# Performance work log

Hardware: AMD Instinct MI355X
Metric: run time of the kernel (lower is better)

Reference implementation:

```python
import jax, jax.numpy as jnp
import numpy as np

N = 65536          # nodes
D = 64             # nclasses / head dim
H = 1              # num_heads (forward math requires H == 1)
NITER = 4
NITER_ATTN = 4
KHOP = 2           # npow_attn(=1, hard-coded) + 1
R = 1024           # row-chunk size in residual loss
DEG = 8            # out-degree before symmetrization


def setup_inputs():
    rng = np.random.default_rng(0)
    cols0 = rng.integers(0, N, size=N * DEG).astype(np.int32)
    rows0 = np.repeat(np.arange(N, dtype=np.int32), DEG)
    loop = np.arange(N, dtype=np.int32)
    rows = np.concatenate([rows0, cols0, loop])           # symmetrized + self-loops (A + I)
    cols = np.concatenate([cols0, rows0, loop])
    deg = np.bincount(rows, minlength=N).astype(np.float32)
    vals = (1.0 / np.sqrt(deg[rows] * deg[cols])).astype(np.float32)  # D^-1/2 (A+I) D^-1/2
    key = jax.random.key(0)
    ks = jax.random.split(key, 8)
    sc = 1.0 / np.sqrt(D)
    return {
        "local_preds": jax.random.normal(ks[0], (N, D), jnp.float32),
        "idx": jnp.arange(N, dtype=jnp.int32),
        "adj_rows": jnp.asarray(rows),
        "adj_cols": jnp.asarray(cols),
        "adj_vals": jnp.asarray(vals),
        "Wq_w": jax.random.normal(ks[1], (H * D, D), jnp.float32) * sc,
        "Wq_b": jax.random.normal(ks[2], (H * D,), jnp.float32) * sc,
        "Wk_w": jax.random.normal(ks[3], (H * D, D), jnp.float32) * sc,
        "Wk_b": jax.random.normal(ks[4], (H * D,), jnp.float32) * sc,
        "lin1_w": jax.random.normal(ks[5], (1, NITER), jnp.float32) * sc,
        "lin2_w": jax.random.normal(ks[6], (1, NITER_ATTN), jnp.float32) * sc,
    }


def _spmm(rows, cols, vals, x):
    # sparse (A+I)_norm @ x via gather + segment-sum
    return jax.ops.segment_sum(vals[:, None] * x[cols], rows, num_segments=N)


def _fro(x):
    return jnp.sqrt(jnp.sum(x * x))


def _on_attn(qn, kn, vs, n_norm):
    # On_attention_conv with pre-normalized qn/kn, K_hop = KHOP
    new_vs = vs
    for _ in range(KHOP):
        kv = jnp.einsum('lhm,lhd->hmd', kn, new_vs)
        new_vs = jnp.einsum('nhm,hmd->nhd', qn, kv)
    new_vs = new_vs + vs.sum(axis=0)[None]           # + vs_sum broadcast over rows
    normz = jnp.einsum('nhm,hm->nh', qn, kn.sum(axis=0))[..., None] + n_norm
    return new_vs / normz


def _forward(local_preds, adj_rows, adj_cols, adj_vals, Wq_w, Wq_b, Wk_w, Wk_b, lin1_w, lin2_w):
    preds = local_preds
    query = (preds @ Wq_w.T + Wq_b).reshape(N, H, D)
    key_t = (preds @ Wk_w.T + Wk_b).reshape(N, H, D)
    qn = query / _fro(query)   # global-Frobenius normalization (as in torch.norm(qs, p=2))
    kn = key_t / _fro(key_t)
    beta = lin2_w[0]           # [NITER_ATTN]
    alph = lin1_w[0]           # [NITER]

    # main Hop-Stack iteration (H == 1 collapses the head broadcasts)
    M_list = [preds]
    tmp = preds
    for _ in range(1, NITER):
        qk_list = [tmp]
        qk_tmp = tmp
        for _ in range(1, NITER_ATTN):
            qk_tmp = _on_attn(qn, kn, qk_tmp[:, None, :], N).mean(axis=1)
            qk_list.append(qk_tmp)
        mix = jnp.einsum('k,knd->nd', beta, jnp.stack(qk_list))
        tmp = _spmm(adj_rows, adj_cols, adj_vals, mix)
        M_list.append(tmp)
    preds_out = jnp.einsum('k,knd->nd', alph, jnp.stack(M_list))

    # residual loss (torch.no_grad, N > r branch), computed in closed form per row-chunk
    m2 = [query.mean(axis=1)]
    t = query.mean(axis=1)
    for _ in range(2, NITER_ATTN):
        o = _on_attn(qn, kn, t[:, None, :], N).mean(axis=1)
        t = _spmm(adj_rows, adj_cols, adj_vals, o)
        m2.append(t)
    gq = jnp.einsum('k,knd->nd', beta[1:], jnp.stack(m2))[:, None, :]  # GraphA_q [N,H,D]
    c = N // R
    s = jnp.sqrt(jnp.sum(gq.reshape(c, -1) ** 2, axis=1))       # per-chunk Frobenius norm of qs
    row_chunk = jnp.arange(N) // R
    qn2 = gq * (1.0 / s)[row_chunk][:, None, None]
    normz = jnp.einsum('nhm,hm->nh', qn2, kn.sum(axis=0)) + R   # [N,H]
    G = jnp.einsum('lhm,lhp->hmp', kn, kn)                      # key gram [H,D,D]
    # ||attn||_F^2 summed over all chunks, without materializing [R,H,N]
    t1 = jnp.sum(jnp.einsum('nhm,hmp,nhp->nh', qn2, G, qn2) / normz ** 2)
    c0 = beta[0] - 1.0
    dots = jnp.einsum('ehm,ehm->eh', qn2[adj_rows], kn[adj_cols])  # attn at sparse A entries
    t2 = 2.0 * c0 * jnp.sum(adj_vals[:, None] * dots / normz[adj_rows])
    t3 = c0 ** 2 * H * jnp.sum(adj_vals ** 2)
    loss = jnp.sqrt(t1 + t2 + t3)
    return preds_out, jax.lax.stop_gradient(loss)


def reference(local_preds, idx, adj_rows, adj_cols, adj_vals, Wq_w, Wq_b, Wk_w, Wk_b, lin1_w, lin2_w):
    del idx  # unused by the original forward body
    return _forward(local_preds, adj_rows, adj_cols, adj_vals, Wq_w, Wq_b, Wk_w, Wk_b, lin1_w, lin2_w)
```

## Files before the change

### kernel.cpp

```cpp
#include <hip/hip_runtime.h>

#define NN 65536
#define DD 64
#define ND (NN*DD)
#define E0 (NN*8)
#define B1 128
#define EPB (E0/B1)

enum {
  SM_ACC   = 0,
  SM_SCAL  = 4,
  SM_KSUM  = 24,
  SM_CHUNK = 96,
  SM_T2    = 160,
  SM_KQ    = 2208,
  SM_G     = SM_KQ + 4096,
  SM_C0    = SM_G + 4096,
  SM_H     = SM_C0 + 4240,
  SM_Z     = SM_H + 4096,
  SM_ZF    = SM_Z + 4160,
  SM_C     = SM_ZF + 4160,
  SM_CMIX  = SM_C + 4240,
  SM_CFIN  = SM_CMIX + 4240,
  SM_END   = SM_CFIN + 4240
};

#define GP 512
#define RP 512
#define QKP 1024
#define GRAM_STRIDE 12544

__device__ __forceinline__ void f4arr(float4 v, float* a){ a[0]=v.x; a[1]=v.y; a[2]=v.z; a[3]=v.w; }

__device__ __forceinline__ unsigned short f2bf(float f){
  union{float f;unsigned u;}v; v.f=f;
  unsigned r = v.u + 0x7fffu + ((v.u>>16)&1u);
  return (unsigned short)(r>>16);
}
__device__ __forceinline__ float bf2f(unsigned short h){
  union{unsigned u;float f;}v; v.u=((unsigned)h)<<16; return v.f;
}

__global__ __launch_bounds__(256,4) void k_qk(const float* __restrict__ preds,
    const float* __restrict__ Wq, const float* __restrict__ bq,
    const float* __restrict__ Wk, const float* __restrict__ bk,
    float* __restrict__ qout, float* __restrict__ kout, float* __restrict__ slab)
{
  __shared__ float sWq[64*68];
  __shared__ float sWk[64*68];
  __shared__ float sbq[64], sbk[64], sks[64];
  __shared__ float sred[8];
  int t = threadIdx.x;
  for (int i=t;i<4096;i+=256){ int d=i>>6, m=i&63; sWq[m*68+d]=Wq[i]; sWk[m*68+d]=Wk[i]; }
  if (t<64){ sbq[t]=bq[t]; sbk[t]=bk[t]; sks[t]=0.f; }
  __syncthreads();
  int td=t&15, g=t>>4, d0=td*4;
  int base = blockIdx.x*64;
  float aq[16], ak[16];
  #pragma unroll
  for (int i=0;i<4;i++)
    #pragma unroll
    for (int j=0;j<4;j++){ aq[i*4+j]=sbq[d0+j]; ak[i*4+j]=sbk[d0+j]; }
  const float4* pr0=(const float4*)(preds+(size_t)(base+g   )*DD);
  const float4* pr1=(const float4*)(preds+(size_t)(base+g+16)*DD);
  const float4* pr2=(const float4*)(preds+(size_t)(base+g+32)*DD);
  const float4* pr3=(const float4*)(preds+(size_t)(base+g+48)*DD);
  float4 pc0=pr0[0], pc1=pr1[0], pc2=pr2[0], pc3=pr3[0];
  for (int ms=0; ms<16; ms++){
    float4 pn0=pc0,pn1=pc1,pn2=pc2,pn3=pc3;
    if (ms<15){ pn0=pr0[ms+1]; pn1=pr1[ms+1]; pn2=pr2[ms+1]; pn3=pr3[ms+1]; }
    int m=ms*4;
    float wq[4][4], wk[4][4];
    #pragma unroll
    for (int k=0;k<4;k++){ f4arr(*(const float4*)&sWq[(m+k)*68+d0], wq[k]); f4arr(*(const float4*)&sWk[(m+k)*68+d0], wk[k]); }
    float p[4];
    f4arr(pc0,p);
    #pragma unroll
    for (int k=0;k<4;k++)
      #pragma unroll
      for (int j=0;j<4;j++){ aq[0*4+j]+=p[k]*wq[k][j]; ak[0*4+j]+=p[k]*wk[k][j]; }
    f4arr(pc1,p);
    #pragma unroll
    for (int k=0;k<4;k++)
      #pragma unroll
      for (int j=0;j<4;j++){ aq[1*4+j]+=p[k]*wq[k][j]; ak[1*4+j]+=p[k]*wk[k][j]; }
    f4arr(pc2,p);
    #pragma unroll
    for (int k=0;k<4;k++)
      #pragma unroll
      for (int j=0;j<4;j++){ aq[2*4+j]+=p[k]*wq[k][j]; ak[2*4+j]+=p[k]*wk[k][j]; }
    f4arr(pc3,p);
    #pragma unroll
    for (int k=0;k<4;k++)
      #pragma unroll
      for (int j=0;j<4;j++){ aq[3*4+j]+=p[k]*wq[k][j]; ak[3*4+j]+=p[k]*wk[k][j]; }
    pc0=pn0; pc1=pn1; pc2=pn2; pc3=pn3;
  }
  float ssq=0.f, ssk=0.f;
  #pragma unroll
  for (int i=0;i<4;i++){
    int r=base+g+16*i;
    float4 Q=make_float4(aq[i*4+0],aq[i*4+1],aq[i*4+2],aq[i*4+3]);
    float4 K=make_float4(ak[i*4+0],ak[i*4+1],ak[i*4+2],ak[i*4+3]);
    ((float4*)(qout+(size_t)r*DD))[td]=Q;
    ((float4*)(kout+(size_t)r*DD))[td]=K;
    ssq += Q.x*Q.x+Q.y*Q.y+Q.z*Q.z+Q.w*Q.w;
    ssk += K.x*K.x+K.y*K.y+K.z*K.z+K.w*K.w;
  }
  #pragma unroll
  for (int j=0;j<4;j++){
    float cs = ak[0*4+j]+ak[1*4+j]+ak[2*4+j]+ak[3*4+j];
    atomicAdd(&sks[d0+j], cs);
  }
  #pragma unroll
  for (int off=32;off;off>>=1){ ssq+=__shfl_down(ssq,off,64); ssk+=__shfl_down(ssk,off,64); }
  if ((t&63)==0){ sred[t>>6]=ssq; sred[4+(t>>6)]=ssk; }
  __syncthreads();
  float* my = slab + (size_t)blockIdx.x*66;
  if (t<64) my[t]=sks[t];
  if (t==0){ my[64]=sred[0]+sred[1]+sred[2]+sred[3]; my[65]=sred[4]+sred[5]+sred[6]+sred[7]; }
}

__global__ __launch_bounds__(256) void k_psumW(const float* __restrict__ slab, int stride, int n, int P,
                                               float* __restrict__ out)
{
  int col=blockIdx.x*4+(threadIdx.x>>6);
  int lane=threadIdx.x&63;
  if (col>=n) return;
  float a0=0.f,a1=0.f;
  int p=lane;
  for (; p+64<P; p+=128){ a0+=slab[(size_t)p*stride+col]; a1+=slab[(size_t)(p+64)*stride+col]; }
  for (; p<P; p+=64) a0+=slab[(size_t)p*stride+col];
  float a=a0+a1;
  #pragma unroll
  for (int off=32;off;off>>=1) a+=__shfl_down(a,off,64);
  if (lane==0) out[col]=a;
}

__global__ void k_scalars(float* __restrict__ ksum, float* __restrict__ sc, const float* __restrict__ lin2){
  __shared__ float s_ki;
  int t=threadIdx.x;
  if (t==0){
    float fq=sqrtf(ksum[64]), fk=sqrtf(ksum[65]);
    float qi=1.f/fq, ki=1.f/fk;
    sc[0]=qi; sc[1]=ki; sc[2]=qi*ki; sc[3]=lin2[1]*qi; sc[4]=1.f;
    sc[5]=ki;    sc[6]=1.f; sc[7]=qi;
    sc[8]=qi*ki; sc[9]=qi;  sc[10]=qi;
    s_ki=ki;
  }
  __syncthreads();
  if (t<64) ksum[t]*=s_ki;
}

__global__ __launch_bounds__(256) void k_gramc0p(const float* __restrict__ qn, const float* __restrict__ kn,
    const float* __restrict__ ksum, const float* __restrict__ sc,
    float* __restrict__ invn, float* __restrict__ slab)
{
  __shared__ float sk[16][64], sq[16][64], sw[16], sks[64];
  int t=threadIdx.x, tp=t&15, tm=t>>4;
  if (t<64) sks[t]=ksum[t];
  float qi_=sc[0];
  float akq[16], ag[16], ac0[16];
  #pragma unroll
  for (int i=0;i<16;i++){akq[i]=0.f;ag[i]=0.f;ac0[i]=0.f;}
  float rb[4]={0,0,0,0}, cb[4]={0,0,0,0}; float s22=0.f;
  for (int tile=blockIdx.x; tile<NN/16; tile+=gridDim.x){
    int base=tile*16;
    ((float4*)sk)[t]=((const float4*)(kn+(size_t)base*DD))[t];
    ((float4*)sq)[t]=((const float4*)(qn+(size_t)base*DD))[t];
    __syncthreads();
    {
      float p = sq[tm][tp]*sks[tp] + sq[tm][tp+16]*sks[tp+16]
              + sq[tm][tp+32]*sks[tp+32] + sq[tm][tp+48]*sks[tp+48];
      p += __shfl_xor(p,1,64); p += __shfl_xor(p,2,64);
      p += __shfl_xor(p,4,64); p += __shfl_xor(p,8,64);
      float w = 1.f/(p*qi_ + (float)NN);
      if (tp==0){ sw[tm]=w; invn[base+tm]=w; }
    }
    __syncthreads();
    #pragma unroll
    for (int r=0;r<16;r++){
      float w=sw[r];
      float km[4],qp[4],kp[4];
      f4arr(((const float4*)&sk[r][0])[tm], km);
      f4arr(((const float4*)&sq[r][0])[tp], qp);
      f4arr(((const float4*)&sk[r][0])[tp], kp);
      float wq[4]={w*qp[0],w*qp[1],w*qp[2],w*qp[3]};
      #pragma unroll
      for (int i=0;i<4;i++)
        #pragma unroll
        for (int j=0;j<4;j++){
          akq[i*4+j]+=km[i]*qp[j];
          ag [i*4+j]+=km[i]*kp[j];
          ac0[i*4+j]+=km[i]*wq[j];
        }
      if (tp==0){
        #pragma unroll
        for (int i=0;i<4;i++) rb[i]+=km[i]*w;
      }
      if (tm==0){
        #pragma unroll
        for (int j=0;j<4;j++) cb[j]+=wq[j];
      }
      if (t==0) s22+=w;
    }
    __syncthreads();
  }
  float* my = slab + (size_t)blockIdx.x*GRAM_STRIDE;
  #pragma unroll
  for (int i=0;i<4;i++)
    #pragma unroll
    for (int j=0;j<4;j++){
      my[       (tm*4+i)*DD+tp*4+j] = akq[i*4+j];
      my[4096 + (tm*4+i)*DD+tp*4+j] = ag [i*4+j];
      my[8192 + (tm*4+i)*65+tp*4+j] = ac0[i*4+j];
    }
  if (tp==0){
    #pragma unroll
    for (int i=0;i<4;i++) my[8192 + (tm*4+i)*65+64] = rb[i];
  }
  if (tm==0){
    #pragma unroll
    for (int j=0;j<4;j++) my[8192 + 64*65+tp*4+j] = cb[j];
  }
  if (t==0) my[8192 + 64*65+64] = s22;
}

__global__ void k_applyscale(float* __restrict__ KQ, float* __restrict__ G, float* __restrict__ C0,
                             const float* __restrict__ sc){
  int i=blockIdx.x*256+threadIdx.x;
  float qi=sc[0], ki=sc[1], qk=sc[2];
  if (i<4096){ KQ[i]*=qk; G[i]*=ki*ki; }
  if (i<4225){
    int a=i/65, b=i-65*a;
    float s = (a<64)? (b<64? qk : ki) : (b<64? qi : 1.f);
    C0[i]*=s;
  }
}

__global__ __launch_bounds__(256) void k_Hp(const float* __restrict__ q2, const float* __restrict__ wv,
                                            float* __restrict__ slab)
{
  __shared__ float sq[16][64], sw[16];
  int t=threadIdx.x, tp=t&15, tm=t>>4;
  float acc[16];
  #pragma unroll
  for (int i=0;i<16;i++) acc[i]=0.f;
  for (int tile=blockIdx.x; tile<NN/16; tile+=gridDim.x){
    int base=tile*16;
    ((float4*)sq)[t]=((const float4*)(q2+(size_t)base*DD))[t];
    if (t<16) sw[t]=wv[base+t];
    __syncthreads();
    #pragma unroll
    for (int r=0;r<16;r++){
      float w=sw[r]; w=w*w;
      float qm[4],qp[4];
      f4arr(((const float4*)&sq[r][0])[tm], qm);
      f4arr(((const float4*)&sq[r][0])[tp], qp);
      float wq[4]={w*qp[0],w*qp[1],w*qp[2],w*qp[3]};
      #pragma unroll
      for (int i=0;i<4;i++)
        #pragma unroll
        for (int j=0;j<4;j++) acc[i*4+j]+=qm[i]*wq[j];
    }
    __syncthreads();
  }
  float* my = slab + (size_t)blockIdx.x*4096;
  #pragma unroll
  for (int i=0;i<4;i++)
    #pragma unroll
    for (int j=0;j<4;j++) my[(tm*4+i)*DD+tp*4+j] = acc[i*4+j];
}

__global__ __launch_bounds__(256) void k_redp(const float* __restrict__ kn, const float* __restrict__ v,
                                              float* __restrict__ slab)
{
  __shared__ float sk[16][64], sv[16][64];
  int t=threadIdx.x, tp=t&15, tm=t>>4;
  float acc[16];
  #pragma unroll
  for (int i=0;i<16;i++) acc[i]=0.f;
  float cs[4]={0,0,0,0};
  for (int tile=blockIdx.x; tile<NN/16; tile+=gridDim.x){
    int base=tile*16;
    ((float4*)sk)[t]=((const float4*)(kn+(size_t)base*DD))[t];
    ((float4*)sv)[t]=((const float4*)(v+(size_t)base*DD))[t];
    __syncthreads();
    #pragma unroll
    for (int r=0;r<16;r++){
      float km[4],vd[4];
      f4arr(((const float4*)&sk[r][0])[tm], km);
      f4arr(((const float4*)&sv[r][0])[tp], vd);
      #pragma unroll
      for (int i=0;i<4;i++)
        #pragma unroll
        for (int j=0;j<4;j++) acc[i*4+j]+=km[i]*vd[j];
      if (tm==0){
        #pragma unroll
        for (int j=0;j<4;j++) cs[j]+=vd[j];
      }
    }
    __syncthreads();
  }
  float* my = slab + (size_t)blockIdx.x*4160;
  #pragma unroll
  for (int i=0;i<4;i++)
    #pragma unroll
    for (int j=0;j<4;j++) my[(tm*4+i)*DD+tp*4+j] = acc[i*4+j];
  if (tm==0){
    #pragma unroll
    for (int j=0;j<4;j++) my[64*DD+tp*4+j] = cs[j];
  }
}

__global__ void k_zfin(const float* __restrict__ Cfin, const float* __restrict__ z, float* __restrict__ zf,
                       const float* __restrict__ sc3){
  int a=blockIdx.x, d=threadIdx.x;
  float it=sc3[0], ib=sc3[1], ot=sc3[2];
  float acc=0.f;
  for (int b=0;b<64;b++) acc += Cfin[a*65+b]*z[b*DD+d];
  acc = acc*it + Cfin[a*65+64]*ib*z[64*DD+d];
  zf[a*DD+d] = (a<64? ot:1.f)*acc;
}
__global__ void k_zB(const float* __restrict__ KQ, const float* __restrict__ z, float* __restrict__ zf,
                     const float* __restrict__ sc3){
  int a=blockIdx.x, d=threadIdx.x;
  float it=sc3[0], ib=sc3[1], ot=sc3[2];
  float acc;
  if (a<64){ acc=0.f; for (int m=0;m<64;m++) acc += KQ[a*DD+m]*z[m*DD+d]; acc*=it*ot; }
  else acc = ib*z[64*DD+d];
  zf[a*DD+d]=acc;
}

__global__ __launch_bounds__(256) void k_expand(const float* __restrict__ qn,
    const float* __restrict__ Zf, const float* __restrict__ invn, const float* __restrict__ sdeg,
    const float* __restrict__ self, const float* __restrict__ coefp, int cidx,
    unsigned short* __restrict__ outv)
{
  __shared__ float sQ[64*68];
  __shared__ float sZ[65*64];
  int t=threadIdx.x;
  int base=blockIdx.x*64;
  for (int i=t;i<1040;i+=256) ((float4*)sZ)[i]=((const float4*)Zf)[i];
  for (int i=t;i<1024;i+=256){
    int r=i>>4, c4=i&15;
    float4 v=((const float4*)(qn+(size_t)(base+r)*DD))[c4];
    float* dst=&sQ[r*68+c4*4]; dst[0]=v.x;dst[1]=v.y;dst[2]=v.z;dst[3]=v.w;
  }
  __syncthreads();
  int td=t&15, g=t>>4, d0=td*4;
  float acc[16];
  {
    float ones[4]; f4arr(*(const float4*)&sZ[64*DD+d0], ones);
    #pragma unroll
    for (int i=0;i<4;i++)
      #pragma unroll
      for (int j=0;j<4;j++) acc[i*4+j]=ones[j];
  }
  #pragma unroll 2
  for (int m=0;m<64;m+=4){
    float zr[4][4];
    #pragma unroll
    for (int k=0;k<4;k++) f4arr(*(const float4*)&sZ[(m+k)*DD+d0], zr[k]);
    #pragma unroll
    for (int i=0;i<4;i++){
      float p[4]; f4arr(*(const float4*)&sQ[(g+16*i)*68+m], p);
      #pragma unroll
      for (int k=0;k<4;k++)
        #pragma unroll
        for (int j=0;j<4;j++) acc[i*4+j]+=p[k]*zr[k][j];
    }
  }
  bool hasself=(cidx>=0);
  float cc = hasself ? coefp[cidx] : 0.f;
  #pragma unroll
  for (int i=0;i<4;i++){
    int r=base+g+16*i;
    float w=invn[r];
    float sd=sdeg[r];
    float4 o=make_float4(acc[i*4+0]*w,acc[i*4+1]*w,acc[i*4+2]*w,acc[i*4+3]*w);
    if (hasself){
      float4 s4=((const float4*)(self+(size_t)r*DD))[td];
      o.x+=cc*s4.x; o.y+=cc*s4.y; o.z+=cc*s4.z; o.w+=cc*s4.w;
    }
    o.x*=sd; o.y*=sd; o.z*=sd; o.w*=sd;
    ushort4 o4; o4.x=f2bf(o.x); o4.y=f2bf(o.y); o4.z=f2bf(o.z); o4.w=f2bf(o.w);
    ((ushort4*)(outv+(size_t)r*DD))[td]=o4;
  }
}

__global__ void k_makeC(const float* __restrict__ C0, const float* __restrict__ KQ, float* __restrict__ C){
  int a=blockIdx.x, d=threadIdx.x;
  float acc=0.f;
  for (int m=0;m<64;m++) acc += C0[a*65+m]*KQ[m*DD+d];
  C[a*65+d]=acc;
  if (d==0) C[a*65+64]=C0[a*65+64];
}
__global__ void k_makeCmix(const float* __restrict__ C, const float* __restrict__ lin2, float* __restrict__ Cmix){
  int a=blockIdx.x, c=threadIdx.x;
  if (c>=65) return;
  float b1=lin2[1], b2=lin2[2], b3=lin2[3];
  float acc=0.f;
  for (int b=0;b<65;b++) acc += C[a*65+b]*C[b*65+c];
  float r = b2*C[a*65+c] + b3*acc;
  if (a==c) r += b1;
  Cmix[a*65+c]=r;
}
__global__ void k_makeCfin(const float* __restrict__ KQ, const float* __restrict__ Cmix, float* __restrict__ Cfin){
  int a=blockIdx.x, c=threadIdx.x;
  if (c>=65) return;
  float acc;
  if (a<64){ acc=0.f; for (int m=0;m<64;m++) acc += KQ[a*DD+m]*Cmix[m*65+c]; }
  else acc = Cmix[64*65+c];
  Cfin[a*65+c]=acc;
}

__global__ __launch_bounds__(256) void k_hist2(const int* __restrict__ acols, unsigned int* __restrict__ slab){
  __shared__ unsigned int lc[16384];
  int t=threadIdx.x;
  for (int i=t;i<16384;i+=256) lc[i]=0u;
  __syncthreads();
  int e0=blockIdx.x*EPB;
  for (int i=t;i<EPB;i+=256){
    int c=acols[e0+i];
    atomicAdd(&lc[c>>2], 1u<<((c&3)*8));
  }
  __syncthreads();
  unsigned int* my=slab+(size_t)blockIdx.x*16384;
  for (int i=t;i<16384;i+=256) my[i]=lc[i];
}

__global__ __launch_bounds__(256) void k_pscan(unsigned int* __restrict__ slab, int* __restrict__ cnt,
                                               float* __restrict__ sdeg, float* __restrict__ accs){
  int w=blockIdx.x*256+threadIdx.x;
  unsigned int r0=0,r1=0,r2=0,r3=0;
  for (int b=0;b<B1;b++){
    unsigned int v=slab[(size_t)b*16384+w];
    slab[(size_t)b*16384+w] = r0|(r1<<8)|(r2<<16)|(r3<<24);
    r0+=v&255u; r1+=(v>>8)&255u; r2+=(v>>16)&255u; r3+=(v>>24)&255u;
  }
  ((int4*)cnt)[w]=make_int4((int)r0,(int)r1,(int)r2,(int)r3);
  float d0=(float)r0+9.f, d1=(float)r1+9.f, d2=(float)r2+9.f, d3=(float)r3+9.f;
  float s0=1.f/sqrtf(d0), s1=1.f/sqrtf(d1), s2=1.f/sqrtf(d2), s3=1.f/sqrtf(d3);
  ((float4*)sdeg)[w]=make_float4(s0,s1,s2,s3);
  float t3 = 1.f/(d0*d0)+1.f/(d1*d1)+1.f/(d2*d2)+1.f/(d3*d3);
  #pragma unroll
  for (int off=32;off;off>>=1) t3+=__shfl_down(t3,off,64);
  if ((threadIdx.x&63)==0) atomicAdd(&accs[1], t3);
}

__global__ __launch_bounds__(1024) void k_scan(const int* __restrict__ cnt, int* __restrict__ row_start){
  __shared__ int wtot[16];
  int t=threadIdx.x, lane=t&63, wid=t>>6;
  int base=t*64;
  int s=0;
  for (int i=0;i<64;i++) s+=cnt[base+i];
  int tot=s;
  for (int off=1;off<64;off<<=1){ int v=__shfl_up(s,off,64); if(lane>=off) s+=v; }
  if (lane==63) wtot[wid]=s;
  __syncthreads();
  if (t<16){
    int v=wtot[t];
    for (int off=1;off<16;off<<=1){ int u=__shfl_up(v,off,64); if(t>=off) v+=u; }
    wtot[t]=v;
  }
  __syncthreads();
  int excl = s - tot + (wid? wtot[wid-1]:0);
  int run=excl;
  for (int i=0;i<64;i++){ row_start[base+i]=run; run+=cnt[base+i]; }
  if (t==1023) row_start[NN]=run;
}

__global__ __launch_bounds__(256) void k_scatter2(const int* __restrict__ acols,
    const unsigned int* __restrict__ slab, const int* __restrict__ row_start,
    const float* __restrict__ sdeg, unsigned short* __restrict__ ccols16, float* __restrict__ accs){
  __shared__ unsigned int lc[16384];
  int t=threadIdx.x;
  for (int i=t;i<16384;i+=256) lc[i]=0u;
  __syncthreads();
  int e0=blockIdx.x*EPB;
  const unsigned int* my=slab+(size_t)blockIdx.x*16384;
  float t3=0.f;
  for (int i=t;i<EPB;i+=256){
    int e=e0+i;
    int c=acols[e];
    unsigned int sh=(unsigned int)(c&3)*8u;
    unsigned int old=atomicAdd(&lc[c>>2], 1u<<sh);
    unsigned int lp=(old>>sh)&255u;
    unsigned int pref=(my[c>>2]>>sh)&255u;
    int slot=row_start[c]+(int)pref+(int)lp;
    ccols16[slot]=(unsigned short)(e>>3);
    float sp=sdeg[e>>3]*sdeg[c];
    t3 += 2.f*sp*sp;
  }
  #pragma unroll
  for (int off=32;off;off>>=1) t3+=__shfl_down(t3,off,64);
  __shared__ float sred[4];
  if ((t&63)==0) sred[t>>6]=t3;
  __syncthreads();
  if (t==0) atomicAdd(&accs[1], sred[0]+sred[1]+sred[2]+sred[3]);
}

__global__ __launch_bounds__(256) void k_spmm2(const int* __restrict__ row_start,
    const unsigned short* __restrict__ ccols16, const int* __restrict__ acols,
    const float* __restrict__ sdeg,
    const unsigned short* __restrict__ xs, float* __restrict__ outv, int wout,
    float* __restrict__ accbuf, const float* __restrict__ coefp, int cidx,
    const float* __restrict__ initsrc, int initc, const float* __restrict__ iscale)
{
  int lane=threadIdx.x&63;
  int row=blockIdx.x*4+(threadIdx.x>>6);
  int s=row_start[row], e=row_start[row+1];
  int din=e-s;
  int dc=din>56?56:din;
  int L=8+dc;
  int myc=0;
  if (lane<8) myc=acols[row*8+lane];
  else if (lane<L) myc=(int)ccols16[s+lane-8];
  float a0=0,a1=0,a2=0,a3=0,a4=0,a5=0,a6=0,a7=0;
  int i=0;
  for (; i+8<=L; i+=8){
    int c0=__shfl(myc,i  ,64), c1=__shfl(myc,i+1,64), c2=__shfl(myc,i+2,64), c3=__shfl(myc,i+3,64);
    int c4=__shfl(myc,i+4,64), c5=__shfl(myc,i+5,64), c6=__shfl(myc,i+6,64), c7=__shfl(myc,i+7,64);
    float v0=bf2f(xs[(size_t)c0*DD+lane]), v1=bf2f(xs[(size_t)c1*DD+lane]);
    float v2=bf2f(xs[(size_t)c2*DD+lane]), v3=bf2f(xs[(size_t)c3*DD+lane]);
    float v4=bf2f(xs[(size_t)c4*DD+lane]), v5=bf2f(xs[(size_t)c5*DD+lane]);
    float v6=bf2f(xs[(size_t)c6*DD+lane]), v7=bf2f(xs[(size_t)c7*DD+lane]);
    a0+=v0; a1+=v1; a2+=v2; a3+=v3; a4+=v4; a5+=v5; a6+=v6; a7+=v7;
  }
  for (; i+4<=L; i+=4){
    int c0=__shfl(myc,i,64), c1=__shfl(myc,i+1,64), c2=__shfl(myc,i+2,64), c3=__shfl(myc,i+3,64);
    a0+=bf2f(xs[(size_t)c0*DD+lane]); a1+=bf2f(xs[(size_t)c1*DD+lane]);
    a2+=bf2f(xs[(size_t)c2*DD+lane]); a3+=bf2f(xs[(size_t)c3*DD+lane]);
  }
  for (; i<L; ++i){
    int c=__shfl(myc,i,64);
    a0 += bf2f(xs[(size_t)c*DD+lane]);
  }
  for (int j=56;j<din;j++){ int c=(int)ccols16[s+j]; a0+=bf2f(xs[(size_t)c*DD+lane]); }
  float acc=((a0+a1)+(a2+a3))+((a4+a5)+(a6+a7));
  acc += bf2f(xs[(size_t)row*DD+lane]);
  acc *= sdeg[row];
  size_t off=(size_t)row*DD+lane;
  if (wout) outv[off]=acc;
  if (cidx>=0){
    float cc=coefp[cidx];
    float base;
    if (initc>=0){
      float isc = iscale ? *iscale : coefp[initc];
      base = isc*initsrc[off];
    } else base = accbuf[off];
    accbuf[off]=base+cc*acc;
  }
}

__global__ __launch_bounds__(256) void k_scalerows(const float4* __restrict__ kn, const float* __restrict__ sdeg,
                                                   const float* __restrict__ sc, unsigned short* __restrict__ kns){
  float ki=sc[1];
  int i=blockIdx.x*256+threadIdx.x;
  int stride=gridDim.x*256;
  for (; i<ND/4; i+=stride){
    float sd=sdeg[i>>4]*ki;
    float4 v=kn[i];
    ushort4 o; o.x=f2bf(sd*v.x); o.y=f2bf(sd*v.y); o.z=f2bf(sd*v.z); o.w=f2bf(sd*v.w);
    ((ushort4*)kns)[i]=o;
  }
}

__global__ __launch_bounds__(256) void k_t2v(const int* __restrict__ row_start,
    const unsigned short* __restrict__ ccols16, const int* __restrict__ acols,
    const float* __restrict__ sdeg, const unsigned short* __restrict__ kns,
    const float* __restrict__ q2, const float* __restrict__ w, float* __restrict__ t2out)
{
  int lane=threadIdx.x&63;
  int wid=blockIdx.x*4+(threadIdx.x>>6);
  int nw=gridDim.x*4;
  float t=0.f;
  for (int row=wid; row<NN; row+=nw){
    int s=row_start[row], e=row_start[row+1];
    int din=e-s;
    int dc=din>56?56:din;
    int L=8+dc;
    int myc=0;
    if (lane<8) myc=acols[row*8+lane];
    else if (lane<L) myc=(int)ccols16[s+lane-8];
    float a0=0,a1=0,a2=0,a3=0,a4=0,a5=0,a6=0,a7=0;
    int i=0;
    for (; i+8<=L; i+=8){
      int c0=__shfl(myc,i  ,64), c1=__shfl(myc,i+1,64), c2=__shfl(myc,i+2,64), c3=__shfl(myc,i+3,64);
      int c4=__shfl(myc,i+4,64), c5=__shfl(myc,i+5,64), c6=__shfl(myc,i+6,64), c7=__shfl(myc,i+7,64);
      a0+=bf2f(kns[(size_t)c0*DD+lane]); a1+=bf2f(kns[(size_t)c1*DD+lane]);
      a2+=bf2f(kns[(size_t)c2*DD+lane]); a3+=bf2f(kns[(size_t)c3*DD+lane]);
      a4+=bf2f(kns[(size_t)c4*DD+lane]); a5+=bf2f(kns[(size_t)c5*DD+lane]);
      a6+=bf2f(kns[(size_t)c6*DD+lane]); a7+=bf2f(kns[(size_t)c7*DD+lane]);
    }
    for (; i+4<=L; i+=4){
      int c0=__shfl(myc,i,64), c1=__shfl(myc,i+1,64), c2=__shfl(myc,i+2,64), c3=__shfl(myc,i+3,64);
      a0+=bf2f(kns[(size_t)c0*DD+lane]); a1+=bf2f(kns[(size_t)c1*DD+lane]);
      a2+=bf2f(kns[(size_t)c2*DD+lane]); a3+=bf2f(kns[(size_t)c3*DD+lane]);
    }
    for (; i<L; ++i){
      int c=__shfl(myc,i,64);
      a0 += bf2f(kns[(size_t)c*DD+lane]);
    }
    for (int j=56;j<din;j++){ int c=(int)ccols16[s+j]; a0+=bf2f(kns[(size_t)c*DD+lane]); }
    float acc=((a0+a1)+(a2+a3))+((a4+a5)+(a6+a7));
    acc += bf2f(kns[(size_t)row*DD+lane]);
    t += w[row]*q2[(size_t)row*DD+lane]*sdeg[row]*acc;
  }
  #pragma unroll
  for (int off=32;off;off>>=1) t+=__shfl_down(t,off,64);
  __shared__ float sred[4];
  if ((threadIdx.x&63)==0) sred[threadIdx.x>>6]=t;
  __syncthreads();
  if (threadIdx.x==0) t2out[blockIdx.x]=sred[0]+sred[1]+sred[2]+sred[3];
}

__global__ __launch_bounds__(256) void k_chunk(const float* __restrict__ gq, float* __restrict__ chunk_inv){
  int c=blockIdx.x;
  const float4* p=(const float4*)(gq + (size_t)c*65536);
  float ss=0.f;
  for (int i=threadIdx.x;i<16384;i+=256){ float4 v=p[i]; ss += v.x*v.x+v.y*v.y+v.z*v.z+v.w*v.w; }
  __shared__ float red[4];
  #pragma unroll
  for (int off=32;off;off>>=1) ss+=__shfl_down(ss,off,64);
  if ((threadIdx.x&63)==0) red[threadIdx.x>>6]=ss;
  __syncthreads();
  if (threadIdx.x==0){ float s=red[0]+red[1]+red[2]+red[3]; chunk_inv[c]=1.f/sqrtf(s); }
}

__global__ __launch_bounds__(256) void k_nrm2(float* __restrict__ gq, const float* __restrict__ chunk_inv,
                                              const float* __restrict__ ks, float* __restrict__ nrm2inv){
  __shared__ float sks[64];
  if (threadIdx.x<64) sks[threadIdx.x]=ks[threadIdx.x];
  __syncthreads();
  int lane=threadIdx.x&63;
  int wid=blockIdx.x*4+(threadIdx.x>>6);
  int nw=gridDim.x*4;
  for (int row=wid;row<NN;row+=nw){
    float q=gq[(size_t)row*DD+lane]*chunk_inv[row>>10];
    gq[(size_t)row*DD+lane]=q;
    float p=q*sks[lane];
    #pragma unroll
    for (int off=32;off;off>>=1) p+=__shfl_down(p,off,64);
    if (lane==0) nrm2inv[row]=1.f/(p+1024.f);
  }
}

__global__ void k_final(const float* __restrict__ G, const float* __restrict__ H,
                        const float* __restrict__ t2s, const float* __restrict__ accs,
                        const float* __restrict__ lin2, float* __restrict__ outv){
  __shared__ float red[256];
  __shared__ float gh;
  int t=threadIdx.x;
  float s=0.f;
  for (int i=t;i<4096;i+=256) s+=G[i]*H[i];
  red[t]=s;
  __syncthreads();
  for (int k=128;k;k>>=1){ if (t<k) red[t]+=red[t+k]; __syncthreads(); }
  if (t==0) gh=red[0];
  __syncthreads();
  float s2=0.f;
  for (int i=t;i<2048;i+=256) s2+=t2s[i];
  red[t]=s2;
  __syncthreads();
  for (int k=128;k;k>>=1){ if (t<k) red[t]+=red[t+k]; __syncthreads(); }
  if (t==0){
    float c0=lin2[0]-1.f;
    outv[0]=sqrtf(gh + 2.f*c0*red[0] + c0*c0*accs[1]);
  }
}

extern "C" void kernel_launch(void* const* d_in, const int* in_sizes, int n_in,
                              void* d_out, int out_size, void* d_ws, size_t ws_size,
                              hipStream_t stream)
{
  (void)n_in; (void)out_size; (void)ws_size; (void)in_sizes;
  const float* preds = (const float*)d_in[0];
  const int*   acols = (const int*)d_in[3];
  const float* Wq    = (const float*)d_in[5];
  const float* bq    = (const float*)d_in[6];
  const float* Wk    = (const float*)d_in[7];
  const float* bk    = (const float*)d_in[8];
  const float* lin1  = (const float*)d_in[9];
  const float* lin2  = (const float*)d_in[10];
  float* outp = (float*)d_out;

  float* W    = (float*)d_ws;
  float* q    = W;
  float* k    = W + (size_t)ND;
  float* tmpM = W + 2*(size_t)ND;
  unsigned short* mixh = (unsigned short*)(W + 3*(size_t)ND);
  float* bufv = W + 3*(size_t)ND + ND/2;
  float* invn = bufv + (size_t)ND;
  float* sdeg = invn + NN;
  float* sm   = sdeg + NN;
  int* cnt       = (int*)(sm + SM_END);
  int* row_start = cnt + NN;
  unsigned short* ccols16 = (unsigned short*)(row_start + NN + 1);
  float* slab = (float*)(ccols16 + E0);

  unsigned int* hist_slab = (unsigned int*)tmpM;
  unsigned short* knsh = mixh;

  float* sc=sm+SM_SCAL;
  float* KQ=sm+SM_KQ; float* G=sm+SM_G; float* H=sm+SM_H;
  float* z=sm+SM_Z; float* zf=sm+SM_ZF;
  float* C0=sm+SM_C0; float* C=sm+SM_C; float* Cmix=sm+SM_CMIX; float* Cfin=sm+SM_CFIN;

  hipMemsetAsync(sm, 0, 24*sizeof(float), stream);

  k_qk<<<QKP,256,0,stream>>>(preds,Wq,bq,Wk,bk,q,k,slab);
  k_psumW<<<(66+3)/4,256,0,stream>>>(slab, 66, 66, QKP, sm+SM_KSUM);
  k_scalars<<<1,64,0,stream>>>(sm+SM_KSUM, sc, lin2);
  k_gramc0p<<<GP,256,0,stream>>>(q,k,sm+SM_KSUM,sc,invn,slab);
  k_psumW<<<(12417+3)/4,256,0,stream>>>(slab, GRAM_STRIDE, 12417, GP, KQ);
  k_applyscale<<<17,256,0,stream>>>(KQ,G,C0,sc);
  k_makeC<<<65,64,0,stream>>>(C0,KQ,C);
  k_makeCmix<<<65,128,0,stream>>>(C,lin2,Cmix);
  k_makeCfin<<<65,128,0,stream>>>(KQ,Cmix,Cfin);

  k_hist2<<<B1,256,0,stream>>>(acols, hist_slab);
  k_pscan<<<64,256,0,stream>>>(hist_slab, cnt, sdeg, sm+SM_ACC);
  k_scan<<<1,1024,0,stream>>>(cnt, row_start);
  k_scatter2<<<B1,256,0,stream>>>(acols, hist_slab, row_start, sdeg, ccols16, sm+SM_ACC);

  for (int i=1;i<4;i++){
    const float* v = (i==1) ? preds : tmpM;
    k_redp<<<RP,256,0,stream>>>(k,v,slab);
    k_psumW<<<(4160+3)/4,256,0,stream>>>(slab, 4160, 4160, RP, z);
    k_zfin<<<65,64,0,stream>>>(Cfin,z,zf, sc+5);
    k_expand<<<1024,256,0,stream>>>(q,zf,invn,sdeg,v,lin2,0,mixh);
    if (i==1)
      k_spmm2<<<16384,256,0,stream>>>(row_start,ccols16,acols,sdeg,mixh,tmpM,1,outp,lin1,1,preds,0,nullptr);
    else
      k_spmm2<<<16384,256,0,stream>>>(row_start,ccols16,acols,sdeg,mixh,tmpM,1,outp,lin1,i,nullptr,-1,nullptr);
  }

  k_redp<<<RP,256,0,stream>>>(k,q,slab);
  k_psumW<<<(4160+3)/4,256,0,stream>>>(slab, 4160, 4160, RP, z);
  k_zB<<<65,64,0,stream>>>(KQ,z,zf, sc+8);
  k_expand<<<1024,256,0,stream>>>(q,zf,invn,sdeg,nullptr,nullptr,-1,mixh);
  k_spmm2<<<16384,256,0,stream>>>(row_start,ccols16,acols,sdeg,mixh,bufv,1,tmpM,lin2,2,q,1,sc+3);
  k_redp<<<RP,256,0,stream>>>(k,bufv,slab);
  k_psumW<<<(4160+3)/4,256,0,stream>>>(slab, 4160, 4160, RP, z);
  k_zB<<<65,64,0,stream>>>(KQ,z,zf, sc+5);
  k_expand<<<1024,256,0,stream>>>(q,zf,invn,sdeg,nullptr,nullptr,-1,mixh);
  k_spmm2<<<16384,256,0,stream>>>(row_start,ccols16,acols,sdeg,mixh,nullptr,0,tmpM,lin2,3,nullptr,-1,nullptr);

  k_chunk<<<64,256,0,stream>>>(tmpM, sm+SM_CHUNK);
  k_nrm2<<<2048,256,0,stream>>>(tmpM, sm+SM_CHUNK, sm+SM_KSUM, invn);
  k_scalerows<<<1024,256,0,stream>>>((const float4*)k, sdeg, sc, knsh);
  k_Hp<<<RP,256,0,stream>>>(tmpM, invn, slab);
  k_psumW<<<(4096+3)/4,256,0,stream>>>(slab, 4096, 4096, RP, H);
  k_t2v<<<2048,256,0,stream>>>(row_start,ccols16,acols,sdeg,knsh,tmpM,invn,sm+SM_T2);
  k_final<<<1,256,0,stream>>>(G,H,sm+SM_T2,sm+SM_ACC,lin2,outp+ND);
}
```

Measured before the change: 694.2 us.

## Store per-block partial reduction slabs in bf16 and double reduction grid sizes

Per-block partial sums from the gram, z-reduction and H kernels are now written to the scratch slab as packed bf16 instead of fp32, and a new bf16-reading column-sum kernel folds them. The grid sizes for these partial-reduction kernels are roughly doubled (512 to about 1008/1024 blocks) to raise occupancy, and the C0 layout is padded to a 68 stride so it can take vector stores. The q-dot for the normalizer is computed from registers instead of shared memory, which removes one barrier. Rounding each partial to bf16 before summing over about a thousand partials adds precision error to the loss and attention matrices.

New measurement: 708.0 us. No clear change (+2.0%).

```diff
diff --git a/kernel.cpp b/kernel.cpp
--- a/kernel.cpp
+++ b/kernel.cpp
@@ -16,7 +16,7 @@
   SM_KQ    = 2208,
   SM_G     = SM_KQ + 4096,
   SM_C0    = SM_G + 4096,
-  SM_H     = SM_C0 + 4240,
+  SM_H     = SM_C0 + 4420,
   SM_Z     = SM_H + 4096,
   SM_ZF    = SM_Z + 4160,
   SM_C     = SM_ZF + 4160,
@@ -25,10 +25,10 @@
   SM_END   = SM_CFIN + 4240
 };
 
-#define GP 512
-#define RP 512
+#define GP 1008
+#define RP 1024
 #define QKP 1024
-#define GRAM_STRIDE 12544
+#define GSTRIDE 12616
 
 __device__ __forceinline__ void f4arr(float4 v, float* a){ a[0]=v.x; a[1]=v.y; a[2]=v.z; a[3]=v.w; }
 
@@ -39,6 +39,9 @@
 }
 __device__ __forceinline__ float bf2f(unsigned short h){
   union{unsigned u;float f;}v; v.u=((unsigned)h)<<16; return v.f;
+}
+__device__ __forceinline__ ushort4 pk4(float a, float b, float c, float d){
+  ushort4 u; u.x=f2bf(a); u.y=f2bf(b); u.z=f2bf(c); u.w=f2bf(d); return u;
 }
 
 __global__ __launch_bounds__(256,4) void k_qk(const float* __restrict__ preds,
@@ -137,6 +140,22 @@
   if (lane==0) out[col]=a;
 }
 
+__global__ __launch_bounds__(256) void k_psumWH(const unsigned short* __restrict__ slab, int stride, int n, int P,
+                                                float* __restrict__ out)
+{
+  int col=blockIdx.x*4+(threadIdx.x>>6);
+  int lane=threadIdx.x&63;
+  if (col>=n) return;
+  float a0=0.f,a1=0.f;
+  int p=lane;
+  for (; p+64<P; p+=128){ a0+=bf2f(slab[(size_t)p*stride+col]); a1+=bf2f(slab[(size_t)(p+64)*stride+col]); }
+  for (; p<P; p+=64) a0+=bf2f(slab[(size_t)p*stride+col]);
+  float a=a0+a1;
+  #pragma unroll
+  for (int off=32;off;off>>=1) a+=__shfl_down(a,off,64);
+  if (lane==0) out[col]=a;
+}
+
 __global__ void k_scalars(float* __restrict__ ksum, float* __restrict__ sc, const float* __restrict__ lin2){
   __shared__ float s_ki;
   int t=threadIdx.x;
@@ -154,7 +173,7 @@
 
 __global__ __launch_bounds__(256) void k_gramc0p(const float* __restrict__ qn, const float* __restrict__ kn,
     const float* __restrict__ ksum, const float* __restrict__ sc,
-    float* __restrict__ invn, float* __restrict__ slab)
+    float* __restrict__ invn, unsigned short* __restrict__ slab)
 {
   __shared__ float sk[16][64], sq[16][64], sw[16], sks[64];
   int t=threadIdx.x, tp=t&15, tm=t>>4;
@@ -164,18 +183,20 @@
   #pragma unroll
   for (int i=0;i<16;i++){akq[i]=0.f;ag[i]=0.f;ac0[i]=0.f;}
   float rb[4]={0,0,0,0}, cb[4]={0,0,0,0}; float s22=0.f;
+  int srow=t>>4, scol=(t&15)*4;
   for (int tile=blockIdx.x; tile<NN/16; tile+=gridDim.x){
     int base=tile*16;
     ((float4*)sk)[t]=((const float4*)(kn+(size_t)base*DD))[t];
-    ((float4*)sq)[t]=((const float4*)(qn+(size_t)base*DD))[t];
-    __syncthreads();
+    float4 qv=((const float4*)(qn+(size_t)base*DD))[t];
+    ((float4*)sq)[t]=qv;
     {
-      float p = sq[tm][tp]*sks[tp] + sq[tm][tp+16]*sks[tp+16]
-              + sq[tm][tp+32]*sks[tp+32] + sq[tm][tp+48]*sks[tp+48];
+      float p = qv.x*sks[scol] + qv.y*sks[scol+1] + qv.z*sks[scol+2] + qv.w*sks[scol+3];
       p += __shfl_xor(p,1,64); p += __shfl_xor(p,2,64);
       p += __shfl_xor(p,4,64); p += __shfl_xor(p,8,64);
-      float w = 1.f/(p*qi_ + (float)NN);
-      if (tp==0){ sw[tm]=w; invn[base+tm]=w; }
+      if ((t&15)==0){
+        float w = 1.f/(p*qi_ + (float)NN);
+        sw[srow]=w; invn[base+srow]=w;
+      }
     }
     __syncthreads();
     #pragma unroll
@@ -206,24 +227,22 @@
     }
     __syncthreads();
   }
-  float* my = slab + (size_t)blockIdx.x*GRAM_STRIDE;
-  #pragma unroll
-  for (int i=0;i<4;i++)
-    #pragma unroll
-    for (int j=0;j<4;j++){
-      my[       (tm*4+i)*DD+tp*4+j] = akq[i*4+j];
-      my[4096 + (tm*4+i)*DD+tp*4+j] = ag [i*4+j];
-      my[8192 + (tm*4+i)*65+tp*4+j] = ac0[i*4+j];
-    }
+  unsigned short* my = slab + (size_t)blockIdx.x*GSTRIDE;
+  #pragma unroll
+  for (int i=0;i<4;i++){
+    int a=tm*4+i;
+    *(ushort4*)(my +        a*DD + tp*4) = pk4(akq[i*4+0],akq[i*4+1],akq[i*4+2],akq[i*4+3]);
+    *(ushort4*)(my + 4096 + a*DD + tp*4) = pk4(ag [i*4+0],ag [i*4+1],ag [i*4+2],ag [i*4+3]);
+    *(ushort4*)(my + 8192 + a*68 + tp*4) = pk4(ac0[i*4+0],ac0[i*4+1],ac0[i*4+2],ac0[i*4+3]);
+  }
   if (tp==0){
     #pragma unroll
-    for (int i=0;i<4;i++) my[8192 + (tm*4+i)*65+64] = rb[i];
+    for (int i=0;i<4;i++) my[8192 + (tm*4+i)*68 + 64] = f2bf(rb[i]);
   }
   if (tm==0){
-    #pragma unroll
-    for (int j=0;j<4;j++) my[8192 + 64*65+tp*4+j] = cb[j];
-  }
-  if (t==0) my[8192 + 64*65+64] = s22;
+    *(ushort4*)(my + 8192 + 64*68 + tp*4) = pk4(cb[0],cb[1],cb[2],cb[3]);
+  }
+  if (t==0) my[8192 + 64*68 + 64] = f2bf(s22);
 }
 
 __global__ void k_applyscale(float* __restrict__ KQ, float* __restrict__ G, float* __restrict__ C0,
@@ -231,15 +250,15 @@
   int i=blockIdx.x*256+threadIdx.x;
   float qi=sc[0], ki=sc[1], qk=sc[2];
   if (i<4096){ KQ[i]*=qk; G[i]*=ki*ki; }
-  if (i<4225){
-    int a=i/65, b=i-65*a;
+  if (i<4420){
+    int a=i/68, b=i-68*a;
     float s = (a<64)? (b<64? qk : ki) : (b<64? qi : 1.f);
     C0[i]*=s;
   }
 }
 
 __global__ __launch_bounds__(256) void k_Hp(const float* __restrict__ q2, const float* __restrict__ wv,
-                                            float* __restrict__ slab)
+                                            unsigned short* __restrict__ slab)
 {
   __shared__ float sq[16][64], sw[16];
   int t=threadIdx.x, tp=t&15, tm=t>>4;
@@ -265,15 +284,14 @@
     }
     __syncthreads();
   }
-  float* my = slab + (size_t)blockIdx.x*4096;
+  unsigned short* my = slab + (size_t)blockIdx.x*4096;
   #pragma unroll
   for (int i=0;i<4;i++)
-    #pragma unroll
-    for (int j=0;j<4;j++) my[(tm*4+i)*DD+tp*4+j] = acc[i*4+j];
+    *(ushort4*)(my + (tm*4+i)*DD + tp*4) = pk4(acc[i*4+0],acc[i*4+1],acc[i*4+2],acc[i*4+3]);
 }
 
 __global__ __launch_bounds__(256) void k_redp(const float* __restrict__ kn, const float* __restrict__ v,
-                                              float* __restrict__ slab)
+                                              unsigned short* __restrict__ slab)
 {
   __shared__ float sk[16][64], sv[16][64];
   int t=threadIdx.x, tp=t&15, tm=t>>4;
@@ -302,14 +320,12 @@
     }
     __syncthreads();
   }
-  float* my = slab + (size_t)blockIdx.x*4160;
+  unsigned short* my = slab + (size_t)blockIdx.x*4160;
   #pragma unroll
   for (int i=0;i<4;i++)
-    #pragma unroll
-    for (int j=0;j<4;j++) my[(tm*4+i)*DD+tp*4+j] = acc[i*4+j];
+    *(ushort4*)(my + (tm*4+i)*DD + tp*4) = pk4(acc[i*4+0],acc[i*4+1],acc[i*4+2],acc[i*4+3]);
   if (tm==0){
-    #pragma unroll
-    for (int j=0;j<4;j++) my[64*DD+tp*4+j] = cs[j];
+    *(ushort4*)(my + 64*DD + tp*4) = pk4(cs[0],cs[1],cs[2],cs[3]);
   }
 }
 
@@ -392,9 +408,9 @@
 __global__ void k_makeC(const float* __restrict__ C0, const float* __restrict__ KQ, float* __restrict__ C){
   int a=blockIdx.x, d=threadIdx.x;
   float acc=0.f;
-  for (int m=0;m<64;m++) acc += C0[a*65+m]*KQ[m*DD+d];
+  for (int m=0;m<64;m++) acc += C0[a*68+m]*KQ[m*DD+d];
   C[a*65+d]=acc;
-  if (d==0) C[a*65+64]=C0[a*65+64];
+  if (d==0) C[a*65+64]=C0[a*68+64];
 }
 __global__ void k_makeCmix(const float* __restrict__ C, const float* __restrict__ lin2, float* __restrict__ Cmix){
   int a=blockIdx.x, c=threadIdx.x;
@@ -699,6 +715,7 @@
   int* row_start = cnt + NN;
   unsigned short* ccols16 = (unsigned short*)(row_start + NN + 1);
   float* slab = (float*)(ccols16 + E0);
+  unsigned short* slab16 = (unsigned short*)slab;
 
   unsigned int* hist_slab = (unsigned int*)tmpM;
   unsigned short* knsh = mixh;
@@ -713,9 +730,9 @@
   k_qk<<<QKP,256,0,stream>>>(preds,Wq,bq,Wk,bk,q,k,slab);
   k_psumW<<<(66+3)/4,256,0,stream>>>(slab, 66, 66, QKP, sm+SM_KSUM);
   k_scalars<<<1,64,0,stream>>>(sm+SM_KSUM, sc, lin2);
-  k_gramc0p<<<GP,256,0,stream>>>(q,k,sm+SM_KSUM,sc,invn,slab);
-  k_psumW<<<(12417+3)/4,256,0,stream>>>(slab, GRAM_STRIDE, 12417, GP, KQ);
-  k_applyscale<<<17,256,0,stream>>>(KQ,G,C0,sc);
+  k_gramc0p<<<GP,256,0,stream>>>(q,k,sm+SM_KSUM,sc,invn,slab16);
+  k_psumWH<<<(12612+3)/4,256,0,stream>>>(slab16, GSTRIDE, 12612, GP, KQ);
+  k_applyscale<<<18,256,0,stream>>>(KQ,G,C0,sc);
   k_makeC<<<65,64,0,stream>>>(C0,KQ,C);
   k_makeCmix<<<65,128,0,stream>>>(C,lin2,Cmix);
   k_makeCfin<<<65,128,0,stream>>>(KQ,Cmix,Cfin);
@@ -727,8 +744,8 @@
 
   for (int i=1;i<4;i++){
     const float* v = (i==1) ? preds : tmpM;
-    k_redp<<<RP,256,0,stream>>>(k,v,slab);
-    k_psumW<<<(4160+3)/4,256,0,stream>>>(slab, 4160, 4160, RP, z);
+    k_redp<<<RP,256,0,stream>>>(k,v,slab16);
+    k_psumWH<<<(4160+3)/4,256,0,stream>>>(slab16, 4160, 4160, RP, z);
     k_zfin<<<65,64,0,stream>>>(Cfin,z,zf, sc+5);
     k_expand<<<1024,256,0,stream>>>(q,zf,invn,sdeg,v,lin2,0,mixh);
     if (i==1)
@@ -737,13 +754,13 @@
       k_spmm2<<<16384,256,0,stream>>>(row_start,ccols16,acols,sdeg,mixh,tmpM,1,outp,lin1,i,nullptr,-1,nullptr);
   }
 
-  k_redp<<<RP,256,0,stream>>>(k,q,slab);
-  k_psumW<<<(4160+3)/4,256,0,stream>>>(slab, 4160, 4160, RP, z);
+  k_redp<<<RP,256,0,stream>>>(k,q,slab16);
+  k_psumWH<<<(4160+3)/4,256,0,stream>>>(slab16, 4160, 4160, RP, z);
   k_zB<<<65,64,0,stream>>>(KQ,z,zf, sc+8);
   k_expand<<<1024,256,0,stream>>>(q,zf,invn,sdeg,nullptr,nullptr,-1,mixh);
   k_spmm2<<<16384,256,0,stream>>>(row_start,ccols16,acols,sdeg,mixh,bufv,1,tmpM,lin2,2,q,1,sc+3);
-  k_redp<<<RP,256,0,stream>>>(k,bufv,slab);
-  k_psumW<<<(4160+3)/4,256,0,stream>>>(slab, 4160, 4160, RP, z);
+  k_redp<<<RP,256,0,stream>>>(k,bufv,slab16);
+  k_psumWH<<<(4160+3)/4,256,0,stream>>>(slab16, 4160, 4160, RP, z);
   k_zB<<<65,64,0,stream>>>(KQ,z,zf, sc+5);
   k_expand<<<1024,256,0,stream>>>(q,zf,invn,sdeg,nullptr,nullptr,-1,mixh);
   k_spmm2<<<16384,256,0,stream>>>(row_start,ccols16,acols,sdeg,mixh,nullptr,0,tmpM,lin2,3,nullptr,-1,nullptr);
@@ -751,8 +768,8 @@
   k_chunk<<<64,256,0,stream>>>(tmpM, sm+SM_CHUNK);
   k_nrm2<<<2048,256,0,stream>>>(tmpM, sm+SM_CHUNK, sm+SM_KSUM, invn);
   k_scalerows<<<1024,256,0,stream>>>((const float4*)k, sdeg, sc, knsh);
-  k_Hp<<<RP,256,0,stream>>>(tmpM, invn, slab);
-  k_psumW<<<(4096+3)/4,256,0,stream>>>(slab, 4096, 4096, RP, H);
+  k_Hp<<<RP,256,0,stream>>>(tmpM, invn, slab16);
+  k_psumWH<<<(4096+3)/4,256,0,stream>>>(slab16, 4096, 4096, RP, H);
   k_t2v<<<2048,256,0,stream>>>(row_start,ccols16,acols,sdeg,knsh,tmpM,invn,sm+SM_T2);
   k_final<<<1,256,0,stream>>>(G,H,sm+SM_T2,sm+SM_ACC,lin2,outp+ND);
 }
```
